# Kernel tuning notes

Measured on AMD Instinct MI355X. Metric: run time of the kernel, lower is better.

## Reference

```python
import math
import jax, jax.numpy as jnp
import numpy as np

EMB = 1024
NHEADS = 16
CTX = 2048
LN_EPS = 1e-5


def new_gelu(x):
    c = math.sqrt(2.0 / math.pi)
    return 0.5 * x * (1.0 + jnp.tanh(c * (x + 0.044715 * x * x * x)))


def layer_norm(x, g, b):
    mu = jnp.mean(x, axis=-1, keepdims=True)
    var = jnp.mean(jnp.square(x - mu), axis=-1, keepdims=True)
    return (x - mu) * jax.lax.rsqrt(var + LN_EPS) * g + b


def setup_inputs() -> dict:
    key = jax.random.key(0)
    ks = jax.random.split(key, 12)
    s = 0.02
    return {
        "x": jax.random.normal(ks[0], (2, 2048, EMB), dtype=jnp.float32),
        "ln1_g": jnp.ones((EMB,), jnp.float32),
        "ln1_b": jnp.zeros((EMB,), jnp.float32),
        "W_attn": jax.random.normal(ks[1], (EMB, 3 * EMB), jnp.float32) * s,
        "b_attn": jnp.zeros((3 * EMB,), jnp.float32),
        "W_attn_proj": jax.random.normal(ks[2], (EMB, EMB), jnp.float32) * s,
        "b_attn_proj": jnp.zeros((EMB,), jnp.float32),
        "ln2_g": jnp.ones((EMB,), jnp.float32),
        "ln2_b": jnp.zeros((EMB,), jnp.float32),
        "W_fc": jax.random.normal(ks[3], (EMB, 4 * EMB), jnp.float32) * s,
        "b_fc": jnp.zeros((4 * EMB,), jnp.float32),
        "W_mlp_proj": jax.random.normal(ks[4], (4 * EMB, EMB), jnp.float32) * s,
        "b_mlp_proj": jnp.zeros((EMB,), jnp.float32),
    }


def reference(x, ln1_g, ln1_b, W_attn, b_attn, W_attn_proj, b_attn_proj,
              ln2_g, ln2_b, W_fc, b_fc, W_mlp_proj, b_mlp_proj):
    B, S, E = x.shape
    hd = E // NHEADS

    # x = ln_1(x)
    x = layer_norm(x, ln1_g, ln1_b)

    # attention on normalized x
    qkv = x @ W_attn + b_attn                      # [B,S,3E]
    q, k, v = jnp.split(qkv, 3, axis=-1)
    q = q.reshape(B, S, NHEADS, hd).transpose(0, 2, 1, 3)  # [B,H,S,hd]
    k = k.reshape(B, S, NHEADS, hd).transpose(0, 2, 1, 3)
    v = v.reshape(B, S, NHEADS, hd).transpose(0, 2, 1, 3)

    attn = jnp.einsum("bhqd,bhkd->bhqk", q, k) * (1.0 / math.sqrt(hd))
    causal = jnp.tril(jnp.ones((S, S), dtype=bool))
    attn = jnp.where(causal[None, None], attn, -jnp.inf)
    attn = jax.nn.softmax(attn, axis=-1)
    out = jnp.einsum("bhqk,bhkd->bhqd", attn, v)   # [B,H,S,hd]
    out = out.transpose(0, 2, 1, 3).reshape(B, S, E)
    out = out @ W_attn_proj + b_attn_proj

    x = x + out

    # x = ln_2(x)
    x = layer_norm(x, ln2_g, ln2_b)

    # MLP on normalized x
    h = new_gelu(x @ W_fc + b_fc)
    h = h @ W_mlp_proj + b_mlp_proj
    return x + h
```

## Files before the change

kernel.cpp:

```cpp
#include <hip/hip_runtime.h>
#include <cstdint>

typedef __attribute__((ext_vector_type(8))) short bf16x8;
typedef __attribute__((ext_vector_type(4))) float f32x4;
typedef __attribute__((ext_vector_type(4))) unsigned short u16x4;
typedef unsigned short u16;

#define LOG2E 1.44269504088896340736f

__device__ __forceinline__ u16 f2bf(float f) {
  unsigned u = __builtin_bit_cast(unsigned, f);
  u += 0x7FFFu + ((u >> 16) & 1u);
  return (u16)(u >> 16);
}
__device__ __forceinline__ float bf2f(u16 h) {
  return __builtin_bit_cast(float, ((unsigned)h) << 16);
}

#define GLOAD_LDS16(g, l)                                                              \
  __builtin_amdgcn_global_load_lds((const __attribute__((address_space(1))) void*)(g), \
                                   (__attribute__((address_space(3))) void*)(l), 16, 0, 0)

__global__ __launch_bounds__(256) void k_transpose_bf16(
    const float* __restrict__ W, u16* __restrict__ Wt, int K, int N) {
  __shared__ float tile[32][33];
  const int tid = threadIdx.x;
  const int tx = tid & 31, ty = tid >> 5;
  const int n0 = blockIdx.x * 32, k0 = blockIdx.y * 32;
#pragma unroll
  for (int i = 0; i < 32; i += 8)
    tile[ty + i][tx] = W[(size_t)(k0 + ty + i) * N + n0 + tx];
  __syncthreads();
#pragma unroll
  for (int i = 0; i < 32; i += 8)
    Wt[(size_t)(n0 + ty + i) * K + k0 + tx] = f2bf(tile[tx][ty + i]);
}

__global__ __launch_bounds__(256) void k_layernorm_bf16(
    const float* __restrict__ x, const float* __restrict__ g,
    const float* __restrict__ b, u16* __restrict__ y) {
  const int row = blockIdx.x, tid = threadIdx.x;
  const float4 v = ((const float4*)(x + (size_t)row * 1024))[tid];
  float s = v.x + v.y + v.z + v.w;
#pragma unroll
  for (int m = 1; m < 64; m <<= 1) s += __shfl_xor(s, m);
  __shared__ float ps[8];
  if ((tid & 63) == 0) ps[tid >> 6] = s;
  __syncthreads();
  const float mean = (ps[0] + ps[1] + ps[2] + ps[3]) * (1.0f / 1024.0f);
  const float d0 = v.x - mean, d1 = v.y - mean, d2 = v.z - mean, d3 = v.w - mean;
  float s2 = d0 * d0 + d1 * d1 + d2 * d2 + d3 * d3;
#pragma unroll
  for (int m = 1; m < 64; m <<= 1) s2 += __shfl_xor(s2, m);
  if ((tid & 63) == 0) ps[4 + (tid >> 6)] = s2;
  __syncthreads();
  const float var = (ps[4] + ps[5] + ps[6] + ps[7]) * (1.0f / 1024.0f);
  const float rstd = rsqrtf(var + 1e-5f);
  const float4 gv = ((const float4*)g)[tid];
  const float4 bv = ((const float4*)b)[tid];
  u16x4 o;
  o[0] = f2bf(d0 * rstd * gv.x + bv.x);
  o[1] = f2bf(d1 * rstd * gv.y + bv.y);
  o[2] = f2bf(d2 * rstd * gv.z + bv.z);
  o[3] = f2bf(d3 * rstd * gv.w + bv.w);
  *(u16x4*)(y + (size_t)row * 1024 + tid * 4) = o;
}

__device__ __forceinline__ float gelu_f(float x) {
  const float u = 0.7978845608028654f * (x + 0.044715f * x * x * x);
  const float e = exp2f(u * 2.8853900817779268f);
  const float t = 1.0f - 2.0f / (e + 1.0f);
  return 0.5f * x * (1.0f + t);
}

template <int EPI>
__global__ __launch_bounds__(256, 2) void k_gemm_bt(
    const u16* __restrict__ A, const u16* __restrict__ Bt,
    const float* __restrict__ bias, const u16* __restrict__ resid,
    void* __restrict__ out, u16* __restrict__ vt, int M, int N, int K) {
  __shared__ u16 As[128 * 64];
  __shared__ u16 Bs[128 * 64];
  const int tid = threadIdx.x;
  const int rowBase = blockIdx.y * 128, colBase = blockIdx.x * 128;
  const int w = tid >> 6, l = tid & 63;
  const int wm = w >> 1, wn = w & 1;
  const int lrow = l & 15, lg = l >> 4;
  const int srow = tid >> 3, sslot = tid & 7;

  const f32x4 fz = {0.f, 0.f, 0.f, 0.f};
  f32x4 acc[4][4];
#pragma unroll
  for (int m = 0; m < 4; m++)
#pragma unroll
    for (int n = 0; n < 4; n++) acc[m][n] = fz;

  for (int kt = 0; kt < K; kt += 64) {
#pragma unroll
    for (int i = 0; i < 4; i++) {
      const int r = srow + 32 * i;
      const int gs = sslot ^ (r & 7);
      GLOAD_LDS16(A + (size_t)(rowBase + r) * K + kt + gs * 8, (char*)As + i * 4096 + tid * 16);
      GLOAD_LDS16(Bt + (size_t)(colBase + r) * K + kt + gs * 8, (char*)Bs + i * 4096 + tid * 16);
    }
    __syncthreads();
#pragma unroll
    for (int kc = 0; kc < 2; kc++) {
      bf16x8 av[4], bv[4];
#pragma unroll
      for (int m = 0; m < 4; m++) {
        const int r = wm * 64 + m * 16 + lrow;
        const int sl = (kc * 4 + lg) ^ (r & 7);
        av[m] = *(const bf16x8*)((const char*)As + r * 128 + sl * 16);
      }
#pragma unroll
      for (int n = 0; n < 4; n++) {
        const int r = wn * 64 + n * 16 + lrow;
        const int sl = (kc * 4 + lg) ^ (r & 7);
        bv[n] = *(const bf16x8*)((const char*)Bs + r * 128 + sl * 16);
      }
#pragma unroll
      for (int m = 0; m < 4; m++)
#pragma unroll
        for (int n = 0; n < 4; n++)
          acc[m][n] = __builtin_amdgcn_mfma_f32_16x16x32_bf16(av[m], bv[n], acc[m][n], 0, 0, 0);
    }
    __syncthreads();
  }
#pragma unroll
  for (int n = 0; n < 4; n++) {
    const int col = colBase + wn * 64 + n * 16 + lrow;
    const float bval = bias[col];
#pragma unroll
    for (int m = 0; m < 4; m++) {
      const int row0 = rowBase + wm * 64 + m * 16 + lg * 4;
#pragma unroll
      for (int r = 0; r < 4; r++) {
        const size_t idx = (size_t)(row0 + r) * N + col;
        float v = acc[m][n][r] + bval;
        if (EPI == 0) {
          ((u16*)out)[idx] = f2bf(v);
        } else if (EPI == 2) {
          ((u16*)out)[idx] = f2bf(gelu_f(v));
        } else {
          v += bf2f(resid[idx]);
          ((float*)out)[idx] = v;
        }
      }
    }
  }
}

template <int EPI>
__global__ __launch_bounds__(512, 2) void k_gemm8(
    const u16* __restrict__ A, const u16* __restrict__ Bt,
    const float* __restrict__ bias, void* __restrict__ out,
    u16* __restrict__ vt, int M, int N, int K, int nbx) {
  extern __shared__ char sm[];
  char* smA = sm;
  char* smB = sm + 65536;
  const int tid = threadIdx.x;
  const int q8 = gridDim.x >> 3;
  const int wg = (blockIdx.x & 7) * q8 + (blockIdx.x >> 3);
  const int bx = wg % nbx, by = wg / nbx;
  const int rowBase = by * 256, colBase = bx * 256;
  const int w = tid >> 6, l = tid & 63;
  const int wm = w >> 2, wn = w & 3;
  const int lrow = l & 15, lg = l >> 4;

  const int sArow = tid >> 3;
  const int gsA = (tid & 7) ^ (sArow & 7);
  const int sBrow = tid >> 2;
  const int gsB = (tid & 3) ^ ((tid >> 3) & 3);
  const u16* Ag = A + (size_t)(rowBase + sArow) * K + gsA * 8;
  const u16* Bg = Bt + (size_t)(colBase + sBrow) * K + gsB * 8;

#define STAGE_A8(buf, half, kt)                                                         \
  do {                                                                                  \
    GLOAD_LDS16(Ag + ((size_t)(half)*128) * K + (kt)*64,                                \
                smA + (buf)*32768 + (half)*16384 + tid * 16);                           \
    GLOAD_LDS16(Ag + ((size_t)(half)*128 + 64) * K + (kt)*64,                           \
                smA + (buf)*32768 + (half)*16384 + 8192 + tid * 16);                    \
  } while (0)
#define STAGE_B8(buf, ksl, kt)                                                          \
  do {                                                                                  \
    GLOAD_LDS16(Bg + (size_t)(kt)*64 + (ksl)*32,                                        \
                smB + (buf)*32768 + (ksl)*16384 + tid * 16);                            \
    GLOAD_LDS16(Bg + (size_t)128 * K + (kt)*64 + (ksl)*32,                              \
                smB + (buf)*32768 + (ksl)*16384 + 8192 + tid * 16);                     \
  } while (0)

  const int physB = lg ^ ((lrow >> 1) & 3);

  const f32x4 fz = {0.f, 0.f, 0.f, 0.f};
  f32x4 acc[8][4];
#pragma unroll
  for (int m = 0; m < 8; m++)
#pragma unroll
    for (int n = 0; n < 4; n++) acc[m][n] = fz;

  const int NT = K >> 6;
  STAGE_A8(0, 0, 0);
  STAGE_A8(0, 1, 0);
  STAGE_B8(0, 0, 0);
  STAGE_B8(0, 1, 0);

  for (int kt = 0; kt < NT; ++kt) {
    const int buf = kt & 1, nb = buf ^ 1, nxt = kt + 1;
    const bool pf = nxt < NT;
    const char* Ab = smA + buf * 32768 + wm * 16384;
    const char* Bb = smB + buf * 32768;

    asm volatile("s_waitcnt vmcnt(2)" ::: "memory");
    __builtin_amdgcn_s_barrier();

    bf16x8 a0[4], a1[4], b0[4], b1[4];
#pragma unroll
    for (int i = 0; i < 4; i++) {
      const int r = i * 16 + lrow;
      a0[i] = *(const bf16x8*)(Ab + r * 128 + ((lg) ^ (r & 7)) * 16);
    }
#pragma unroll
    for (int i = 0; i < 4; i++) {
      const int r = wn * 64 + i * 16 + lrow;
      b0[i] = *(const bf16x8*)(Bb + r * 64 + physB * 16);
    }
    if (pf) STAGE_A8(nb, 0, nxt);
    __builtin_amdgcn_s_setprio(1);
#pragma unroll
    for (int m = 0; m < 4; m++)
#pragma unroll
      for (int n = 0; n < 4; n++)
        acc[m][n] = __builtin_amdgcn_mfma_f32_16x16x32_bf16(a0[m], b0[n], acc[m][n], 0, 0, 0);
    __builtin_amdgcn_s_setprio(0);
#pragma unroll
    for (int i = 0; i < 4; i++) {
      const int r = (4 + i) * 16 + lrow;
      a1[i] = *(const bf16x8*)(Ab + r * 128 + ((lg) ^ (r & 7)) * 16);
    }
    if (pf) STAGE_A8(nb, 1, nxt);
    __builtin_amdgcn_s_setprio(1);
#pragma unroll
    for (int m = 0; m < 4; m++)
#pragma unroll
      for (int n = 0; n < 4; n++)
        acc[4 + m][n] = __builtin_amdgcn_mfma_f32_16x16x32_bf16(a1[m], b0[n], acc[4 + m][n], 0, 0, 0);
    __builtin_amdgcn_s_setprio(0);

    if (pf) {
      asm volatile("s_waitcnt vmcnt(4)" ::: "memory");
    } else {
      asm volatile("s_waitcnt vmcnt(0)" ::: "memory");
    }
    __builtin_amdgcn_s_barrier();

#pragma unroll
    for (int i = 0; i < 4; i++) {
      const int r = i * 16 + lrow;
      a0[i] = *(const bf16x8*)(Ab + r * 128 + ((4 + lg) ^ (r & 7)) * 16);
    }
#pragma unroll
    for (int i = 0; i < 4; i++) {
      const int r = wn * 64 + i * 16 + lrow;
      b1[i] = *(const bf16x8*)(Bb + 16384 + r * 64 + physB * 16);
    }
    if (pf) STAGE_B8(nb, 0, nxt);
    __builtin_amdgcn_s_setprio(1);
#pragma unroll
    for (int m = 0; m < 4; m++)
#pragma unroll
      for (int n = 0; n < 4; n++)
        acc[m][n] = __builtin_amdgcn_mfma_f32_16x16x32_bf16(a0[m], b1[n], acc[m][n], 0, 0, 0);
    __builtin_amdgcn_s_setprio(0);
#pragma unroll
    for (int i = 0; i < 4; i++) {
      const int r = (4 + i) * 16 + lrow;
      a1[i] = *(const bf16x8*)(Ab + r * 128 + ((4 + lg) ^ (r & 7)) * 16);
    }
    if (pf) STAGE_B8(nb, 1, nxt);
    __builtin_amdgcn_s_setprio(1);
#pragma unroll
    for (int m = 0; m < 4; m++)
#pragma unroll
      for (int n = 0; n < 4; n++)
        acc[4 + m][n] = __builtin_amdgcn_mfma_f32_16x16x32_bf16(a1[m], b1[n], acc[4 + m][n], 0, 0, 0);
    __builtin_amdgcn_s_setprio(0);
  }

#pragma unroll
  for (int n = 0; n < 4; n++) {
    const int col = colBase + wn * 64 + n * 16 + lrow;
    const float bval = bias[col];
#pragma unroll
    for (int m = 0; m < 8; m++) {
      const int row0 = rowBase + wm * 128 + m * 16 + lg * 4;
      if (EPI == 3 && col >= 2048) {
        const int c2 = col - 2048;
        const int hh = c2 >> 6, dd = c2 & 63;
        const int bat = row0 >> 11, tok0 = row0 & 2047;
        u16x4 pk;
#pragma unroll
        for (int r = 0; r < 4; r++) pk[r] = f2bf(acc[m][n][r] + bval);
        *(u16x4*)(vt + ((size_t)(bat * 16 + hh) * 64 + dd) * 2048 + tok0) = pk;
      } else if (EPI == 3) {
#pragma unroll
        for (int r = 0; r < 4; r++)
          ((u16*)out)[(size_t)(row0 + r) * 2048 + col] = f2bf(acc[m][n][r] + bval);
      } else if (EPI == 2) {
#pragma unroll
        for (int r = 0; r < 4; r++)
          ((u16*)out)[(size_t)(row0 + r) * N + col] = f2bf(gelu_f(acc[m][n][r] + bval));
      } else {
#pragma unroll
        for (int r = 0; r < 4; r++)
          ((u16*)out)[(size_t)(row0 + r) * N + col] = f2bf(acc[m][n][r] + bval);
      }
    }
  }
#undef STAGE_A8
#undef STAGE_B8
}

__global__ __launch_bounds__(256, 2) void k_attention(
    const u16* __restrict__ qk, const u16* __restrict__ VT, u16* __restrict__ out) {
  const int S = 2048, E2 = 2048;
  const int bid = blockIdx.x;
  const int pid = bid >> 5;
  const int bh = bid & 31;
  const int bat = bh >> 4, h = bh & 15;
  const u16* base = qk + (size_t)bat * S * E2;
  const u16* kbase = base + 1024 + h * 64;
  const u16* vbase = VT + (size_t)bh * 64 * S;
  const int tid = threadIdx.x, w = tid >> 6, l = tid & 63;
  const int lrow = l & 15, lg = l >> 4;
  __shared__ u16 Ks[2][64 * 64];
  __shared__ u16 Vs[2][64 * 64];
  __shared__ u16 Pl[4][16 * 64];
  u16* Plw = Pl[w];
  const int srow = tid >> 3, sslot = tid & 7;
  const int gs = sslot ^ (srow & 7);
  const float sc = 0.125f * LOG2E;
  const f32x4 fz = {0.f, 0.f, 0.f, 0.f};

  auto STAGE = [&](int bufi, int kb) {
#pragma unroll
    for (int round = 0; round < 2; round++) {
      const int r = srow + 32 * round;
      GLOAD_LDS16(kbase + (size_t)(kb + r) * E2 + gs * 8, (char*)Ks[bufi] + round * 4096 + tid * 16);
      GLOAD_LDS16(vbase + (size_t)r * S + kb + gs * 8, (char*)Vs[bufi] + round * 4096 + tid * 16);
    }
  };

  for (int pass = 0; pass < 2; ++pass) {
    const int qt = pass ? (31 - pid) : pid;
    const int qrow0 = qt * 64 + w * 16;
    const int nkt = qt + 1;

    bf16x8 qfrag[2];
#pragma unroll
    for (int kc = 0; kc < 2; kc++)
      qfrag[kc] = *(const bf16x8*)(base + (size_t)(qrow0 + lrow) * E2 + h * 64 + kc * 32 + lg * 8);

    f32x4 o[4];
    float mrow[4], lsum[4];
#pragma unroll
    for (int r = 0; r < 4; r++) { mrow[r] = -1e30f; lsum[r] = 0.f; }
#pragma unroll
    for (int df = 0; df < 4; df++) o[df] = fz;

    STAGE(0, 0);
    __syncthreads();

    for (int kt = 0; kt < nkt; kt++) {
      const int cur = kt & 1;
      const int kb = kt * 64;
      if (kt + 1 < nkt) STAGE(cur ^ 1, kb + 64);
      const u16* Kc = Ks[cur];
      const u16* Vc = Vs[cur];

      f32x4 sv[4];
#pragma unroll
      for (int kf = 0; kf < 4; kf++) sv[kf] = fz;
#pragma unroll
      for (int kc = 0; kc < 2; kc++) {
        bf16x8 kfr[4];
#pragma unroll
        for (int kf = 0; kf < 4; kf++) {
          const int rk = kf * 16 + lrow;
          kfr[kf] = *(const bf16x8*)(Kc + rk * 64 + ((kc * 4 + lg) ^ (rk & 7)) * 8);
        }
#pragma unroll
        for (int kf = 0; kf < 4; kf++)
          sv[kf] = __builtin_amdgcn_mfma_f32_16x16x32_bf16(qfrag[kc], kfr[kf], sv[kf], 0, 0, 0);
      }
#pragma unroll
      for (int kf = 0; kf < 4; kf++)
#pragma unroll
        for (int r = 0; r < 4; r++) sv[kf][r] *= sc;
      if (kt == nkt - 1) {
#pragma unroll
        for (int kf = 0; kf < 4; kf++) {
          const int kg = kb + kf * 16 + lrow;
#pragma unroll
          for (int r = 0; r < 4; r++) {
            const int qg = qrow0 + lg * 4 + r;
            if (kg > qg) sv[kf][r] = -1e30f;
          }
        }
      }
#pragma unroll
      for (int r = 0; r < 4; r++) {
        float mx = fmaxf(fmaxf(sv[0][r], sv[1][r]), fmaxf(sv[2][r], sv[3][r]));
#pragma unroll
        for (int msk = 1; msk < 16; msk <<= 1) mx = fmaxf(mx, __shfl_xor(mx, msk));
        const float mnew = fmaxf(mrow[r], mx);
        const float corr = exp2f(mrow[r] - mnew);
        mrow[r] = mnew;
        lsum[r] *= corr;
#pragma unroll
        for (int df = 0; df < 4; df++) o[df][r] *= corr;
        float rsv = 0.f;
#pragma unroll
        for (int kf = 0; kf < 4; kf++) {
          const float p = exp2f(sv[kf][r] - mnew);
          sv[kf][r] = p;
          rsv += p;
        }
#pragma unroll
        for (int msk = 1; msk < 16; msk <<= 1) rsv += __shfl_xor(rsv, msk);
        lsum[r] += rsv;
      }
#pragma unroll
      for (int kf = 0; kf < 4; kf++)
#pragma unroll
        for (int r = 0; r < 4; r++) {
          const int q = lg * 4 + r;
          *(u16*)((char*)Plw + q * 128 + ((kf * 32 + lrow * 2) ^ ((q & 7) << 4))) = f2bf(sv[kf][r]);
        }
#pragma unroll
      for (int kc = 0; kc < 2; kc++) {
        const bf16x8 pa =
            *(const bf16x8*)((const char*)Plw + lrow * 128 + (((kc * 4 + lg) ^ (lrow & 7)) << 4));
        bf16x8 vb[4];
#pragma unroll
        for (int df = 0; df < 4; df++) {
          const int rd = df * 16 + lrow;
          vb[df] = *(const bf16x8*)(Vc + rd * 64 + ((kc * 4 + lg) ^ (rd & 7)) * 8);
        }
#pragma unroll
        for (int df = 0; df < 4; df++)
          o[df] = __builtin_amdgcn_mfma_f32_16x16x32_bf16(pa, vb[df], o[df], 0, 0, 0);
      }
      __syncthreads();
    }
#pragma unroll
    for (int r = 0; r < 4; r++) {
      const float inv = 1.0f / lsum[r];
      const int qg = qrow0 + lg * 4 + r;
#pragma unroll
      for (int df = 0; df < 4; df++) {
        const int col = h * 64 + df * 16 + lrow;
        out[(size_t)(bat * S + qg) * 1024 + col] = f2bf(o[df][r] * inv);
      }
    }
  }
}

extern "C" void kernel_launch(void* const* d_in, const int* in_sizes, int n_in,
                              void* d_out, int out_size, void* d_ws, size_t ws_size,
                              hipStream_t stream) {
  (void)in_sizes; (void)n_in; (void)out_size; (void)ws_size;
  const float* x      = (const float*)d_in[0];
  const float* ln1_g  = (const float*)d_in[1];
  const float* ln1_b  = (const float*)d_in[2];
  const float* W_attn = (const float*)d_in[3];
  const float* b_attn = (const float*)d_in[4];
  const float* W_proj = (const float*)d_in[5];
  const float* b_proj = (const float*)d_in[6];
  const float* ln2_g  = (const float*)d_in[7];
  const float* ln2_b  = (const float*)d_in[8];
  const float* W_fc   = (const float*)d_in[9];
  const float* b_fc   = (const float*)d_in[10];
  const float* W_mlp  = (const float*)d_in[11];
  const float* b_mlp  = (const float*)d_in[12];

  const int M = 4096;
  char* ws = (char*)d_ws;
  size_t off = 0;
  auto alloc = [&](size_t bytes) {
    void* p = ws + off;
    off += (bytes + 255) & ~(size_t)255;
    return p;
  };
  u16* WattnT = (u16*)alloc((size_t)3072 * 1024 * 2);
  u16* WprojT = (u16*)alloc((size_t)1024 * 1024 * 2);
  u16* WfcT   = (u16*)alloc((size_t)4096 * 1024 * 2);
  u16* WmlpT  = (u16*)alloc((size_t)1024 * 4096 * 2);
  u16* x1     = (u16*)alloc((size_t)M * 1024 * 2);
  u16* qkb    = (u16*)alloc((size_t)M * 2048 * 2);
  u16* VT     = (u16*)alloc((size_t)32 * 64 * 2048 * 2);
  u16* attno  = (u16*)alloc((size_t)M * 1024 * 2);
  float* x2   = (float*)alloc((size_t)M * 1024 * 4);
  u16* x3     = (u16*)alloc((size_t)M * 1024 * 2);
  u16* hbuf   = (u16*)alloc((size_t)M * 4096 * 2);

  static bool attr_done = false;
  if (!attr_done) {
    hipFuncSetAttribute((const void*)k_gemm8<3>, hipFuncAttributeMaxDynamicSharedMemorySize, 131072);
    hipFuncSetAttribute((const void*)k_gemm8<2>, hipFuncAttributeMaxDynamicSharedMemorySize, 131072);
    attr_done = true;
  }

  const dim3 blk(256);
  k_transpose_bf16<<<dim3(3072 / 32, 1024 / 32), blk, 0, stream>>>(W_attn, WattnT, 1024, 3072);
  k_transpose_bf16<<<dim3(1024 / 32, 1024 / 32), blk, 0, stream>>>(W_proj, WprojT, 1024, 1024);
  k_transpose_bf16<<<dim3(4096 / 32, 1024 / 32), blk, 0, stream>>>(W_fc, WfcT, 1024, 4096);
  k_transpose_bf16<<<dim3(1024 / 32, 4096 / 32), blk, 0, stream>>>(W_mlp, WmlpT, 4096, 1024);

  k_layernorm_bf16<<<M, blk, 0, stream>>>(x, ln1_g, ln1_b, x1);
  k_gemm8<3><<<dim3((3072 / 256) * (M / 256)), dim3(512), 131072, stream>>>(
      x1, WattnT, b_attn, qkb, VT, M, 3072, 1024, 3072 / 256);
  k_attention<<<dim3(512), blk, 0, stream>>>(qkb, VT, attno);
  k_gemm_bt<1><<<dim3(1024 / 128, M / 128), blk, 0, stream>>>(attno, WprojT, b_proj, x1, x2, nullptr, M, 1024, 1024);
  k_layernorm_bf16<<<M, blk, 0, stream>>>(x2, ln2_g, ln2_b, x3);
  k_gemm8<2><<<dim3((4096 / 256) * (M / 256)), dim3(512), 131072, stream>>>(
      x3, WfcT, b_fc, hbuf, nullptr, M, 4096, 1024, 4096 / 256);
  k_gemm_bt<1><<<dim3(1024 / 128, M / 128), blk, 0, stream>>>(hbuf, WmlpT, b_mlp, x3, d_out, nullptr, M, 1024, 4096);
}
```

Before: 290.2 us.

## Double-buffer the 128x128 GEMM and issue all gemm8 prefetch stages earlier

The k_gemm_bt kernel gains a second LDS buffer for A and B. It now prefetches the next k-tile with global_load_lds while computing on the current one, using vmcnt waits and raw barriers in place of full __syncthreads. In k_gemm8, all A and B stage loads for the next tile are issued in the first half of the iteration instead of being spread across four points, and the wait count is relaxed to match. k_gemm8's launch bound occupancy hint drops from 2 to 1. This gives the compiler more registers but may lower waves per CU. The change also doubles LDS use in k_gemm_bt, and any mismatch between the vmcnt counts and the number of outstanding loads would risk reading stale data.

```diff
diff --git a/kernel.cpp b/kernel.cpp
--- a/kernel.cpp
+++ b/kernel.cpp
@@ -78,8 +78,8 @@
     const u16* __restrict__ A, const u16* __restrict__ Bt,
     const float* __restrict__ bias, const u16* __restrict__ resid,
     void* __restrict__ out, u16* __restrict__ vt, int M, int N, int K) {
-  __shared__ u16 As[128 * 64];
-  __shared__ u16 Bs[128 * 64];
+  __shared__ u16 As[2][128 * 64];
+  __shared__ u16 Bs[2][128 * 64];
   const int tid = threadIdx.x;
   const int rowBase = blockIdx.y * 128, colBase = blockIdx.x * 128;
   const int w = tid >> 6, l = tid & 63;
@@ -94,15 +94,31 @@
 #pragma unroll
     for (int n = 0; n < 4; n++) acc[m][n] = fz;
 
-  for (int kt = 0; kt < K; kt += 64) {
+  const int NT = K >> 6;
+  auto STAGE = [&](int b, int kt) {
 #pragma unroll
     for (int i = 0; i < 4; i++) {
       const int r = srow + 32 * i;
       const int gs = sslot ^ (r & 7);
-      GLOAD_LDS16(A + (size_t)(rowBase + r) * K + kt + gs * 8, (char*)As + i * 4096 + tid * 16);
-      GLOAD_LDS16(Bt + (size_t)(colBase + r) * K + kt + gs * 8, (char*)Bs + i * 4096 + tid * 16);
-    }
-    __syncthreads();
+      GLOAD_LDS16(A + (size_t)(rowBase + r) * K + kt * 64 + gs * 8,
+                  (char*)As[b] + i * 4096 + tid * 16);
+      GLOAD_LDS16(Bt + (size_t)(colBase + r) * K + kt * 64 + gs * 8,
+                  (char*)Bs[b] + i * 4096 + tid * 16);
+    }
+  };
+
+  STAGE(0, 0);
+  for (int kt = 0; kt < NT; ++kt) {
+    const int buf = kt & 1;
+    if (kt + 1 < NT) {
+      STAGE(buf ^ 1, kt + 1);
+      asm volatile("s_waitcnt vmcnt(8)" ::: "memory");
+    } else {
+      asm volatile("s_waitcnt vmcnt(0)" ::: "memory");
+    }
+    __builtin_amdgcn_s_barrier();
+    const char* Ab = (const char*)As[buf];
+    const char* Bb = (const char*)Bs[buf];
 #pragma unroll
     for (int kc = 0; kc < 2; kc++) {
       bf16x8 av[4], bv[4];
@@ -110,13 +126,13 @@
       for (int m = 0; m < 4; m++) {
         const int r = wm * 64 + m * 16 + lrow;
         const int sl = (kc * 4 + lg) ^ (r & 7);
-        av[m] = *(const bf16x8*)((const char*)As + r * 128 + sl * 16);
+        av[m] = *(const bf16x8*)(Ab + r * 128 + sl * 16);
       }
 #pragma unroll
       for (int n = 0; n < 4; n++) {
         const int r = wn * 64 + n * 16 + lrow;
         const int sl = (kc * 4 + lg) ^ (r & 7);
-        bv[n] = *(const bf16x8*)((const char*)Bs + r * 128 + sl * 16);
+        bv[n] = *(const bf16x8*)(Bb + r * 128 + sl * 16);
       }
 #pragma unroll
       for (int m = 0; m < 4; m++)
@@ -124,7 +140,7 @@
         for (int n = 0; n < 4; n++)
           acc[m][n] = __builtin_amdgcn_mfma_f32_16x16x32_bf16(av[m], bv[n], acc[m][n], 0, 0, 0);
     }
-    __syncthreads();
+    __builtin_amdgcn_s_barrier();
   }
 #pragma unroll
   for (int n = 0; n < 4; n++) {
@@ -151,7 +167,7 @@
 }
 
 template <int EPI>
-__global__ __launch_bounds__(512, 2) void k_gemm8(
+__global__ __launch_bounds__(512, 1) void k_gemm8(
     const u16* __restrict__ A, const u16* __restrict__ Bt,
     const float* __restrict__ bias, void* __restrict__ out,
     u16* __restrict__ vt, int M, int N, int K, int nbx) {
@@ -224,7 +240,10 @@
       const int r = wn * 64 + i * 16 + lrow;
       b0[i] = *(const bf16x8*)(Bb + r * 64 + physB * 16);
     }
-    if (pf) STAGE_A8(nb, 0, nxt);
+    if (pf) {
+      STAGE_A8(nb, 0, nxt);
+      STAGE_A8(nb, 1, nxt);
+    }
     __builtin_amdgcn_s_setprio(1);
 #pragma unroll
     for (int m = 0; m < 4; m++)
@@ -237,7 +256,10 @@
       const int r = (4 + i) * 16 + lrow;
       a1[i] = *(const bf16x8*)(Ab + r * 128 + ((lg) ^ (r & 7)) * 16);
     }
-    if (pf) STAGE_A8(nb, 1, nxt);
+    if (pf) {
+      STAGE_B8(nb, 0, nxt);
+      STAGE_B8(nb, 1, nxt);
+    }
     __builtin_amdgcn_s_setprio(1);
 #pragma unroll
     for (int m = 0; m < 4; m++)
@@ -247,7 +269,7 @@
     __builtin_amdgcn_s_setprio(0);
 
     if (pf) {
-      asm volatile("s_waitcnt vmcnt(4)" ::: "memory");
+      asm volatile("s_waitcnt vmcnt(8)" ::: "memory");
     } else {
       asm volatile("s_waitcnt vmcnt(0)" ::: "memory");
     }
@@ -263,7 +285,6 @@
       const int r = wn * 64 + i * 16 + lrow;
       b1[i] = *(const bf16x8*)(Bb + 16384 + r * 64 + physB * 16);
     }
-    if (pf) STAGE_B8(nb, 0, nxt);
     __builtin_amdgcn_s_setprio(1);
 #pragma unroll
     for (int m = 0; m < 4; m++)
@@ -276,7 +297,6 @@
       const int r = (4 + i) * 16 + lrow;
       a1[i] = *(const bf16x8*)(Ab + r * 128 + ((4 + lg) ^ (r & 7)) * 16);
     }
-    if (pf) STAGE_B8(nb, 1, nxt);
     __builtin_amdgcn_s_setprio(1);
 #pragma unroll
     for (int m = 0; m < 4; m++)
```

After: 273.5 us (median of 2 runs). 5.7% less time.
